# Kernel optimization log

Measured on AMD Instinct MI355X. Metric: run time of the kernel, lower is better.

## Reference

```python
import jax, jax.numpy as jnp
import numpy as np

N, E, E3, DIM = 25000, 50000, 40000, 64


def setup_inputs() -> dict:
    key = jax.random.key(0)
    ks = jax.random.split(key, 16)
    def g(k, shape, scale=0.1):
        return jax.random.normal(k, shape, jnp.float32) * scale
    return {
        "x": jax.random.normal(ks[0], (N, 8), jnp.float32),
        "edge_attr": jax.random.uniform(ks[1], (E, 19), dtype=jnp.float32),
        "edge_attr3": jax.random.uniform(ks[2], (E3, 8), dtype=jnp.float32),
        "edge_index": jax.random.randint(ks[3], (2, E), 0, N),
        "edge_index3": jax.random.randint(ks[4], (2, E3), 0, N),
        "W_node": g(ks[5], (8, DIM)), "b_node": jnp.zeros((DIM,), jnp.float32),
        "W_ea": g(ks[6], (19, 12)), "b_ea": jnp.zeros((12,), jnp.float32),
        "W_e1": g(ks[7], (12, 128)), "b_e1": jnp.zeros((128,), jnp.float32),
        "W_e2": g(ks[8], (128, DIM * DIM), 0.01), "b_e2": jnp.zeros((DIM * DIM,), jnp.float32),
        "conv_bias": jnp.zeros((DIM,), jnp.float32),
        "W_ih": g(ks[9], (3 * DIM, DIM)), "b_ih": jnp.zeros((3 * DIM,), jnp.float32),
        "W_hh": g(ks[10], (3 * DIM, DIM)), "b_hh": jnp.zeros((3 * DIM,), jnp.float32),
        "W_l1": g(ks[11], (DIM + 8, 128)), "b_l1": jnp.zeros((128,), jnp.float32),
        "W_l2": g(ks[12], (128, 1)), "b_l2": jnp.zeros((1,), jnp.float32),
    }


def _forward(x, edge_attr, edge_attr3,
             W_node, b_node, W_ea, b_ea, W_e1, b_e1, W_e2, b_e2, conv_bias,
             W_ih, b_ih, W_hh, b_hh, W_l1, b_l1, W_l2, b_l2,
             edge_index, edge_index3):
    dim = W_node.shape[1]
    n = x.shape[0]
    out = jax.nn.relu(x @ W_node + b_node)                      # [N, dim]
    ea = jax.nn.relu(edge_attr @ W_ea + b_ea)                   # [E, 12]
    # edge MLP -> per-edge dim x dim weight matrices (same for all 3 conv calls)
    Wedge = (jax.nn.relu(ea @ W_e1 + b_e1) @ W_e2 + b_e2).reshape(-1, dim, dim)  # [E, dim, dim]
    src, dst = edge_index[0], edge_index[1]
    ones = jnp.ones((src.shape[0],), x.dtype)
    cnt = jnp.maximum(jax.ops.segment_sum(ones, dst, num_segments=n), 1.0)  # [N]
    h = out
    for _ in range(3):
        msg = jnp.einsum('ed,edf->ef', out[src], Wedge)                     # per-edge GEMV
        agg = jax.ops.segment_sum(msg, dst, num_segments=n) / cnt[:, None]  # scatter-mean
        m = jax.nn.relu(agg + conv_bias)
        # single-step GRU (PyTorch gate order: r, z, n)
        gi = m @ W_ih.T + b_ih
        gh = h @ W_hh.T + b_hh
        ir, iz, inn = jnp.split(gi, 3, axis=-1)
        hr, hz, hn = jnp.split(gh, 3, axis=-1)
        r = jax.nn.sigmoid(ir + hr)
        z = jax.nn.sigmoid(iz + hz)
        ng = jnp.tanh(inn + r * hn)
        h = (1.0 - z) * ng + z * h
        out = h
    pair = (out[edge_index3[0]] + out[edge_index3[1]]) * 0.5    # mean over the 2 endpoints
    yhat = jnp.concatenate([pair, edge_attr3], axis=1)          # [E3, dim+8]
    yhat = jax.nn.relu(yhat @ W_l1 + b_l1) @ W_l2 + b_l2        # [E3, 1]
    return yhat[:, 0]


def reference(x, edge_attr, edge_attr3, edge_index, edge_index3,
              W_node, b_node, W_ea, b_ea, W_e1, b_e1, W_e2, b_e2, conv_bias,
              W_ih, b_ih, W_hh, b_hh, W_l1, b_l1, W_l2, b_l2):
    return _forward(x, edge_attr, edge_attr3,
                    W_node, b_node, W_ea, b_ea, W_e1, b_e1, W_e2, b_e2, conv_bias,
                    W_ih, b_ih, W_hh, b_hh, W_l1, b_l1, W_l2, b_l2,
                    edge_index, edge_index3)
```

## Files before the change

kernel.cpp:

```cpp
#include <hip/hip_runtime.h>

typedef unsigned short u16;
typedef unsigned int u32;
typedef __attribute__((ext_vector_type(8))) short short8v;
typedef __attribute__((ext_vector_type(4))) float float4v;

__device__ __forceinline__ float sigm(float x) { return 1.0f / (1.0f + __expf(-x)); }
__device__ __forceinline__ u16 f2bf(float f) {
  u32 u = __float_as_uint(f);
  u32 r = (u + 0x7fffu + ((u >> 16) & 1u)) >> 16;
  return (u16)r;
}
__device__ __forceinline__ float bf2f(u16 w) { return __uint_as_float(((u32)w) << 16); }

__global__ void k_zero_f(float* __restrict__ p, int n) {
  int i = blockIdx.x * blockDim.x + threadIdx.x;
  if (i < n) p[i] = 0.0f;
}
__global__ void k_zero_i(int* __restrict__ p, int n) {
  int i = blockIdx.x * blockDim.x + threadIdx.x;
  if (i < n) p[i] = 0;
}

__global__ void k_cnt(const int* __restrict__ dst, int* __restrict__ cnt, int E) {
  int e = blockIdx.x * blockDim.x + threadIdx.x;
  if (e < E) atomicAdd(&cnt[dst[e]], 1);
}

__global__ void k_node(const float* __restrict__ x, const float* __restrict__ Wn,
                       const float* __restrict__ bn, float* __restrict__ h, int N) {
  int tid = blockIdx.x * blockDim.x + threadIdx.x;
  if (tid >= N * 64) return;
  int n = tid >> 6, f = tid & 63;
  float acc = bn[f];
  for (int k = 0; k < 8; ++k) acc += x[(size_t)n * 8 + k] * Wn[k * 64 + f];
  h[tid] = fmaxf(acc, 0.0f);
}

__global__ __launch_bounds__(256) void k_edge_mlp(
    const float* __restrict__ ea_in, const float* __restrict__ Wea,
    const float* __restrict__ bea, const float* __restrict__ We1,
    const float* __restrict__ be1, u16* __restrict__ Ahi, int E) {
  __shared__ float att[2][19];
  __shared__ float ea[2][12];
  int half = threadIdx.x >> 7;
  int t = threadIdx.x & 127;
  int e = blockIdx.x * 2 + half;
  bool real = (e < E);
  int ee = real ? e : E - 1;
  if (t < 19) att[half][t] = ea_in[(size_t)ee * 19 + t];
  __syncthreads();
  if (t < 12) {
    float a = bea[t];
#pragma unroll
    for (int k = 0; k < 19; ++k) a += att[half][k] * Wea[k * 12 + t];
    ea[half][t] = fmaxf(a, 0.0f);
  }
  __syncthreads();
  float a = be1[t];
#pragma unroll
  for (int j = 0; j < 12; ++j) a += ea[half][j] * We1[j * 128 + t];
  if (real) Ahi[(size_t)e * 128 + t] = f2bf(fmaxf(a, 0.0f));
}

__global__ void k_pack_b(const float* __restrict__ W2, u16* __restrict__ Bph) {
  int tid = blockIdx.x * blockDim.x + threadIdx.x;
  if (tid >= 128 * 4096) return;
  int j = tid & 7;
  int lane = (tid >> 3) & 63;
  int nt = (tid >> 9) & 3;
  int ks = (tid >> 11) & 3;
  int d = tid >> 13;
  int c = lane & 15, q = lane >> 4;
  int k = ks * 32 + q * 8 + j;
  int n = d * 64 + nt * 16 + c;
  Bph[tid] = f2bf(W2[(size_t)k * 4096 + n]);
}

__global__ void k_prep_wtf(const float* __restrict__ Wih, const float* __restrict__ Whh,
                           u16* __restrict__ WpI, u16* __restrict__ WpH) {
  int tid = blockIdx.x * blockDim.x + threadIdx.x;
  if (tid >= 2 * 12288) return;
  int w = tid / 12288;
  int r = tid - w * 12288;
  int jj = r & 7;
  int lane = (r >> 3) & 63;
  int t = r >> 9;
  int nt = t % 12, ks = t / 12;
  int c = lane & 15, q = lane >> 4;
  int j = nt * 16 + c;
  int k = ks * 32 + q * 8 + jj;
  const float* W = w ? Whh : Wih;
  u16* Wp = w ? WpH : WpI;
  Wp[r] = f2bf(W[j * 64 + k]);
}

__global__ void k_prep_wl1(const float* __restrict__ Wl1, u16* __restrict__ Wp1) {
  int tid = blockIdx.x * blockDim.x + threadIdx.x;
  if (tid >= 3 * 8 * 64 * 8) return;
  int j = tid & 7;
  int lane = (tid >> 3) & 63;
  int nt = (tid >> 9) & 7;
  int ks = tid >> 12;
  int c = lane & 15, q = lane >> 4;
  int k = ks * 32 + q * 8 + j;
  int n = nt * 16 + c;
  Wp1[tid] = f2bf((k < 72) ? Wl1[k * 128 + n] : 0.0f);
}

__global__ __launch_bounds__(256, 2) void k_conv_fused(
    const u16* __restrict__ Ahi, const u16* __restrict__ Bph,
    const float* __restrict__ b2, const float* __restrict__ h,
    const int* __restrict__ src, const int* __restrict__ dst,
    float* __restrict__ agg, int E) {
  __shared__ __align__(16) u16 sB[2][8192];
  __shared__ __align__(16) float hs[128 * 36];
  __shared__ __align__(16) float sb2[2048];
  int m0 = blockIdx.x * 128;
  int d0 = blockIdx.y * 32;
  int tid = threadIdx.x;
  int wave = tid >> 6, lane = tid & 63;
  int mw = wave >> 1, fw = wave & 1;
  int c = lane & 15, q = lane >> 4;

  auto stageB = [&](int d, int b) {
    const u16* gp = Bph + (size_t)d * 8192 + wave * 2048 + lane * 8;
    u16* lp = &sB[b][wave * 2048];
#pragma unroll
    for (int i = 0; i < 4; ++i)
      __builtin_amdgcn_global_load_lds(
          (const __attribute__((address_space(1))) unsigned int*)(gp + i * 512),
          (__attribute__((address_space(3))) unsigned int*)(lp + i * 512), 16, 0, 0);
  };

  stageB(d0, 0);

  short8v afr[4][4];
#pragma unroll
  for (int mt = 0; mt < 4; ++mt) {
    int gr = m0 + mw * 64 + mt * 16 + c;
    if (gr >= E) gr = E - 1;
    const u16* ap = Ahi + (size_t)gr * 128 + q * 8;
#pragma unroll
    for (int ks = 0; ks < 4; ++ks) afr[mt][ks] = *(const short8v*)(ap + ks * 32);
  }

#pragma unroll
  for (int p = 0; p < 4; ++p) {
    int slot = p * 256 + tid;
    int r = slot >> 3, s = slot & 7;
    int ge = m0 + r;
    if (ge >= E) ge = E - 1;
    int sn = src[ge];
    *(float4*)(&hs[r * 36 + s * 4]) = *(const float4*)(h + (size_t)sn * 64 + d0 + s * 4);
  }
#pragma unroll
  for (int p = 0; p < 2; ++p) {
    int slot = p * 256 + tid;
    *(float4*)(&sb2[slot * 4]) = *(const float4*)(b2 + d0 * 64 + slot * 4);
  }
  __syncthreads();

  float msg[4][2][4];
#pragma unroll
  for (int mt = 0; mt < 4; ++mt)
#pragma unroll
    for (int nt = 0; nt < 2; ++nt)
#pragma unroll
      for (int r = 0; r < 4; ++r) msg[mt][nt][r] = 0.0f;

  int cur = 0;
  for (int dl = 0; dl < 32; ++dl) {
    if (dl < 31) stageB(d0 + dl + 1, cur ^ 1);
    float4v acc[4][2];
#pragma unroll
    for (int mt = 0; mt < 4; ++mt)
#pragma unroll
      for (int nt = 0; nt < 2; ++nt) acc[mt][nt] = (float4v){0.f, 0.f, 0.f, 0.f};
#pragma unroll
    for (int ks = 0; ks < 4; ++ks) {
      short8v b0 = *(const short8v*)(&sB[cur][ks * 2048 + fw * 1024 + lane * 8]);
      short8v b1 = *(const short8v*)(&sB[cur][ks * 2048 + fw * 1024 + 512 + lane * 8]);
#pragma unroll
      for (int mt = 0; mt < 4; ++mt) {
        acc[mt][0] = __builtin_amdgcn_mfma_f32_16x16x32_bf16(afr[mt][ks], b0, acc[mt][0], 0, 0, 0);
        acc[mt][1] = __builtin_amdgcn_mfma_f32_16x16x32_bf16(afr[mt][ks], b1, acc[mt][1], 0, 0, 0);
      }
    }
#pragma unroll
    for (int mt = 0; mt < 4; ++mt) {
      float hd[4];
#pragma unroll
      for (int r = 0; r < 4; ++r)
        hd[r] = hs[(mw * 64 + mt * 16 + q * 4 + r) * 36 + dl];
#pragma unroll
      for (int nt = 0; nt < 2; ++nt) {
        float b2v = sb2[dl * 64 + fw * 32 + nt * 16 + c];
#pragma unroll
        for (int r = 0; r < 4; ++r) msg[mt][nt][r] += hd[r] * (acc[mt][nt][r] + b2v);
      }
    }
    __syncthreads();
    cur ^= 1;
  }

#pragma unroll
  for (int mt = 0; mt < 4; ++mt) {
#pragma unroll
    for (int r = 0; r < 4; ++r) {
      int e = m0 + mw * 64 + mt * 16 + q * 4 + r;
      if (e < E) {
        int dn = dst[e];
        float* ap = agg + (size_t)dn * 64 + fw * 32 + c;
#pragma unroll
        for (int nt = 0; nt < 2; ++nt) atomicAdd(ap + nt * 16, msg[mt][nt][r]);
      }
    }
  }
}

__global__ __launch_bounds__(256, 2) void k_gru_mfma(
    float* __restrict__ agg, const int* __restrict__ cnt,
    const float* __restrict__ cb, const u16* __restrict__ WpI,
    const u16* __restrict__ WpH, const float* __restrict__ bih,
    const float* __restrict__ bhh, const float* __restrict__ hin,
    float* __restrict__ hout, int N) {
  __shared__ __align__(16) u16 sM[64 * 72];
  __shared__ __align__(16) u16 sH[64 * 72];
  __shared__ __align__(16) float sHf[64 * 68];
  int n0 = blockIdx.x * 64;
  int tid = threadIdx.x;
#pragma unroll
  for (int p = 0; p < 16; ++p) {
    int slot = p * 256 + tid;
    int n = slot >> 6, f = slot & 63;
    int gn = n0 + n;
    bool real = (gn < N);
    if (!real) gn = N - 1;
    float cf = fmaxf((float)cnt[gn], 1.0f);
    float av = agg[(size_t)gn * 64 + f];
    if (real) agg[(size_t)gn * 64 + f] = 0.0f;
    float m = fmaxf(av / cf + cb[f], 0.0f);
    float hv = hin[(size_t)gn * 64 + f];
    sM[n * 72 + f] = f2bf(m);
    sH[n * 72 + f] = f2bf(hv);
    sHf[n * 68 + f] = hv;
  }
  __syncthreads();
  int wave = tid >> 6, lane = tid & 63;
  int c = lane & 15, q = lane >> 4;
  short8v am[2], ah[2];
#pragma unroll
  for (int ks = 0; ks < 2; ++ks) {
    am[ks] = *(const short8v*)(&sM[(wave * 16 + c) * 72 + ks * 32 + q * 8]);
    ah[ks] = *(const short8v*)(&sH[(wave * 16 + c) * 72 + ks * 32 + q * 8]);
  }
  float4v accRZ[8], accN[4], accHN[4];
#pragma unroll
  for (int i = 0; i < 8; ++i) accRZ[i] = (float4v){0.f, 0.f, 0.f, 0.f};
#pragma unroll
  for (int i = 0; i < 4; ++i) {
    accN[i] = (float4v){0.f, 0.f, 0.f, 0.f};
    accHN[i] = (float4v){0.f, 0.f, 0.f, 0.f};
  }
#pragma unroll
  for (int ks = 0; ks < 2; ++ks) {
#pragma unroll
    for (int nt = 0; nt < 8; ++nt) {
      short8v bI = *(const short8v*)(WpI + ((size_t)(ks * 12 + nt) * 64 + lane) * 8);
      short8v bH = *(const short8v*)(WpH + ((size_t)(ks * 12 + nt) * 64 + lane) * 8);
      accRZ[nt] = __builtin_amdgcn_mfma_f32_16x16x32_bf16(am[ks], bI, accRZ[nt], 0, 0, 0);
      accRZ[nt] = __builtin_amdgcn_mfma_f32_16x16x32_bf16(ah[ks], bH, accRZ[nt], 0, 0, 0);
    }
#pragma unroll
    for (int nt = 0; nt < 4; ++nt) {
      short8v bI = *(const short8v*)(WpI + ((size_t)(ks * 12 + 8 + nt) * 64 + lane) * 8);
      short8v bH = *(const short8v*)(WpH + ((size_t)(ks * 12 + 8 + nt) * 64 + lane) * 8);
      accN[nt] = __builtin_amdgcn_mfma_f32_16x16x32_bf16(am[ks], bI, accN[nt], 0, 0, 0);
      accHN[nt] = __builtin_amdgcn_mfma_f32_16x16x32_bf16(ah[ks], bH, accHN[nt], 0, 0, 0);
    }
  }
#pragma unroll
  for (int nt = 0; nt < 4; ++nt) {
    int f = nt * 16 + c;
    float brz_r = bih[f] + bhh[f];
    float brz_z = bih[64 + f] + bhh[64 + f];
    float bin = bih[128 + f];
    float bhn = bhh[128 + f];
#pragma unroll
    for (int r = 0; r < 4; ++r) {
      int nl = wave * 16 + q * 4 + r;
      int gn = n0 + nl;
      float rr = sigm(accRZ[nt][r] + brz_r);
      float zz = sigm(accRZ[nt + 4][r] + brz_z);
      float ng = tanhf(accN[nt][r] + bin + rr * (accHN[nt][r] + bhn));
      float hv = sHf[nl * 68 + f];
      if (gn < N) hout[(size_t)gn * 64 + f] = (1.0f - zz) * ng + zz * hv;
    }
  }
}

__global__ __launch_bounds__(256) void k_final_mfma(
    const float* __restrict__ h, const float* __restrict__ ea3,
    const int* __restrict__ idx3, const u16* __restrict__ Wp1,
    const float* __restrict__ bl1, const float* __restrict__ Wl2,
    const float* __restrict__ bl2, float* __restrict__ out, int E3) {
  __shared__ __align__(16) u16 sF[64 * 104];
  int e0 = blockIdx.x * 64;
  int tid = threadIdx.x;
  {
    int er = tid >> 2;
    int part = tid & 3;
    int ge = e0 + er;
    int gc = (ge < E3) ? ge : E3 - 1;
    int a = idx3[gc], b = idx3[E3 + gc];
    for (int kk = part * 24; kk < part * 24 + 24; ++kk) {
      float v;
      if (kk < 64) v = 0.5f * (h[(size_t)a * 64 + kk] + h[(size_t)b * 64 + kk]);
      else if (kk < 72) v = ea3[(size_t)gc * 8 + (kk - 64)];
      else v = 0.0f;
      sF[er * 104 + kk] = f2bf(v);
    }
  }
  __syncthreads();
  int wave = tid >> 6, lane = tid & 63;
  int c = lane & 15, q = lane >> 4;
  float4v acc[8];
#pragma unroll
  for (int nt = 0; nt < 8; ++nt) acc[nt] = (float4v){0.f, 0.f, 0.f, 0.f};
#pragma unroll
  for (int ks = 0; ks < 3; ++ks) {
    short8v af = *(const short8v*)(&sF[(wave * 16 + c) * 104 + ks * 32 + q * 8]);
#pragma unroll
    for (int nt = 0; nt < 8; ++nt) {
      short8v bf = *(const short8v*)(Wp1 + ((size_t)(ks * 8 + nt) * 64 + lane) * 8);
      acc[nt] = __builtin_amdgcn_mfma_f32_16x16x32_bf16(af, bf, acc[nt], 0, 0, 0);
    }
  }
  float v[4] = {0.f, 0.f, 0.f, 0.f};
#pragma unroll
  for (int nt = 0; nt < 8; ++nt) {
    int n = nt * 16 + c;
    float b1 = bl1[n];
    float w2 = Wl2[n];
#pragma unroll
    for (int r = 0; r < 4; ++r) v[r] += fmaxf(acc[nt][r] + b1, 0.0f) * w2;
  }
#pragma unroll
  for (int off = 1; off < 16; off <<= 1) {
#pragma unroll
    for (int r = 0; r < 4; ++r) v[r] += __shfl_xor(v[r], off);
  }
  if (c == 0) {
    float b2v = bl2[0];
#pragma unroll
    for (int r = 0; r < 4; ++r) {
      int e = e0 + wave * 16 + q * 4 + r;
      if (e < E3) out[e] = v[r] + b2v;
    }
  }
}

extern "C" void kernel_launch(void* const* d_in, const int* in_sizes, int n_in,
                              void* d_out, int out_size, void* d_ws, size_t ws_size,
                              hipStream_t stream) {
  const float* x          = (const float*)d_in[0];
  const float* edge_attr  = (const float*)d_in[1];
  const float* edge_attr3 = (const float*)d_in[2];
  const int*   edge_index = (const int*)d_in[3];
  const int*   edge_index3= (const int*)d_in[4];
  const float* W_node = (const float*)d_in[5];
  const float* b_node = (const float*)d_in[6];
  const float* W_ea   = (const float*)d_in[7];
  const float* b_ea   = (const float*)d_in[8];
  const float* W_e1   = (const float*)d_in[9];
  const float* b_e1   = (const float*)d_in[10];
  const float* W_e2   = (const float*)d_in[11];
  const float* b_e2   = (const float*)d_in[12];
  const float* conv_bias = (const float*)d_in[13];
  const float* W_ih   = (const float*)d_in[14];
  const float* b_ih   = (const float*)d_in[15];
  const float* W_hh   = (const float*)d_in[16];
  const float* b_hh   = (const float*)d_in[17];
  const float* W_l1   = (const float*)d_in[18];
  const float* b_l1   = (const float*)d_in[19];
  const float* W_l2   = (const float*)d_in[20];
  const float* b_l2   = (const float*)d_in[21];

  int N  = in_sizes[0] / 8;
  int E  = in_sizes[1] / 19;
  int E3 = in_sizes[2] / 8;

  char* p = (char*)d_ws;
  auto carve = [&](size_t bytes) -> void* {
    char* q = p;
    p += (bytes + 255) & ~(size_t)255;
    return (void*)q;
  };
  float* hA   = (float*)carve((size_t)N * 64 * 4);
  float* hB   = (float*)carve((size_t)N * 64 * 4);
  float* agg  = (float*)carve((size_t)N * 64 * 4);
  int*   cnt  = (int*)carve((size_t)N * 4);
  u16*   Ahi  = (u16*)carve((size_t)E * 128 * 2);
  u16*   Bph  = (u16*)carve((size_t)128 * 4096 * 2);
  u16*   WpI  = (u16*)carve(12288 * 2);
  u16*   WpH  = (u16*)carve(12288 * 2);
  u16*   Wp1  = (u16*)carve(12288 * 2);

  const int* src = edge_index;
  const int* dst = edge_index + E;

  k_zero_i<<<(N + 255) / 256, 256, 0, stream>>>(cnt, N);
  k_cnt<<<(E + 255) / 256, 256, 0, stream>>>(dst, cnt, E);
  k_node<<<((size_t)N * 64 + 255) / 256, 256, 0, stream>>>(x, W_node, b_node, hA, N);
  k_edge_mlp<<<(E + 1) / 2, 256, 0, stream>>>(edge_attr, W_ea, b_ea, W_e1, b_e1, Ahi, E);
  k_pack_b<<<(128 * 4096 + 255) / 256, 256, 0, stream>>>(W_e2, Bph);
  k_prep_wtf<<<(2 * 12288 + 255) / 256, 256, 0, stream>>>(W_ih, W_hh, WpI, WpH);
  k_prep_wl1<<<(12288 + 255) / 256, 256, 0, stream>>>(W_l1, Wp1);
  k_zero_f<<<((size_t)N * 64 + 255) / 256, 256, 0, stream>>>(agg, N * 64);

  float* hcur = hA;
  float* hnxt = hB;
  dim3 gconv((E + 127) / 128, 2);
  int ngru = (N + 63) / 64;
  for (int it = 0; it < 3; ++it) {
    k_conv_fused<<<gconv, 256, 0, stream>>>(Ahi, Bph, b_e2, hcur, src, dst, agg, E);
    k_gru_mfma<<<ngru, 256, 0, stream>>>(agg, cnt, conv_bias, WpI, WpH,
                                         b_ih, b_hh, hcur, hnxt, N);
    float* tmp = hcur; hcur = hnxt; hnxt = tmp;
  }
  k_final_mfma<<<(E3 + 63) / 64, 256, 0, stream>>>(hcur, edge_attr3, edge_index3, Wp1,
                                                   b_l1, W_l2, b_l2, (float*)d_out, E3);
}
```

Measured before the change: 466.1 us.

## Replace atomic scatter with CSR gather and merge conv d-split blocks

The conv kernel no longer splits the 64 input features across two blocks. Each block now loops over all 64 d slices and writes per-edge messages densely to a message buffer instead of atomically adding into per-node aggregates. A CSR (counting scan plus permutation) built once per call lets the GRU kernel gather and average each node's messages directly, which removes the agg zeroing and the float atomics. In exchange there is an extra E×64 message buffer round trip per iteration and a single-block serial scan. The per-block conv work doubles while the grid halves, and the bias is now stored as bf16 in LDS, which changes the numerics slightly.

```diff
diff --git a/kernel.cpp b/kernel.cpp
--- a/kernel.cpp
+++ b/kernel.cpp
@@ -13,10 +13,6 @@
 }
 __device__ __forceinline__ float bf2f(u16 w) { return __uint_as_float(((u32)w) << 16); }
 
-__global__ void k_zero_f(float* __restrict__ p, int n) {
-  int i = blockIdx.x * blockDim.x + threadIdx.x;
-  if (i < n) p[i] = 0.0f;
-}
 __global__ void k_zero_i(int* __restrict__ p, int n) {
   int i = blockIdx.x * blockDim.x + threadIdx.x;
   if (i < n) p[i] = 0;
@@ -25,6 +21,41 @@
 __global__ void k_cnt(const int* __restrict__ dst, int* __restrict__ cnt, int E) {
   int e = blockIdx.x * blockDim.x + threadIdx.x;
   if (e < E) atomicAdd(&cnt[dst[e]], 1);
+}
+
+__global__ void k_scan(const int* __restrict__ cnt, int* __restrict__ row, int N) {
+  __shared__ int part[256];
+  __shared__ int base[256];
+  int t = threadIdx.x;
+  int chunk = (N + 255) >> 8;
+  int s0 = t * chunk;
+  int s1 = min(s0 + chunk, N);
+  int s = 0;
+  for (int i = s0; i < s1; ++i) s += cnt[i];
+  part[t] = s;
+  __syncthreads();
+  if (t == 0) {
+    int run = 0;
+    for (int i = 0; i < 256; ++i) { int v = part[i]; base[i] = run; run += v; }
+  }
+  __syncthreads();
+  int run = base[t];
+  for (int i = s0; i < s1; ++i) { row[i] = run; run += cnt[i]; }
+  if (t == 255) row[N] = run;
+}
+
+__global__ void k_copy_i(const int* __restrict__ a, int* __restrict__ b, int n) {
+  int i = blockIdx.x * blockDim.x + threadIdx.x;
+  if (i < n) b[i] = a[i];
+}
+
+__global__ void k_perm(const int* __restrict__ dst, int* __restrict__ cursor,
+                       int* __restrict__ perm, int E) {
+  int e = blockIdx.x * blockDim.x + threadIdx.x;
+  if (e < E) {
+    int p = atomicAdd(&cursor[dst[e]], 1);
+    perm[p] = e;
+  }
 }
 
 __global__ void k_node(const float* __restrict__ x, const float* __restrict__ Wn,
@@ -111,13 +142,11 @@
 __global__ __launch_bounds__(256, 2) void k_conv_fused(
     const u16* __restrict__ Ahi, const u16* __restrict__ Bph,
     const float* __restrict__ b2, const float* __restrict__ h,
-    const int* __restrict__ src, const int* __restrict__ dst,
-    float* __restrict__ agg, int E) {
+    const int* __restrict__ src, float* __restrict__ msgout, int E) {
   __shared__ __align__(16) u16 sB[2][8192];
-  __shared__ __align__(16) float hs[128 * 36];
-  __shared__ __align__(16) float sb2[2048];
+  __shared__ __align__(16) float hs[128 * 68];
+  __shared__ __align__(16) u16 sb2h[4096];
   int m0 = blockIdx.x * 128;
-  int d0 = blockIdx.y * 32;
   int tid = threadIdx.x;
   int wave = tid >> 6, lane = tid & 63;
   int mw = wave >> 1, fw = wave & 1;
@@ -133,7 +162,7 @@
           (__attribute__((address_space(3))) unsigned int*)(lp + i * 512), 16, 0, 0);
   };
 
-  stageB(d0, 0);
+  stageB(0, 0);
 
   short8v afr[4][4];
 #pragma unroll
@@ -146,18 +175,24 @@
   }
 
 #pragma unroll
-  for (int p = 0; p < 4; ++p) {
+  for (int p = 0; p < 8; ++p) {
     int slot = p * 256 + tid;
-    int r = slot >> 3, s = slot & 7;
+    int r = slot >> 4, s = slot & 15;
     int ge = m0 + r;
     if (ge >= E) ge = E - 1;
     int sn = src[ge];
-    *(float4*)(&hs[r * 36 + s * 4]) = *(const float4*)(h + (size_t)sn * 64 + d0 + s * 4);
-  }
-#pragma unroll
-  for (int p = 0; p < 2; ++p) {
-    int slot = p * 256 + tid;
-    *(float4*)(&sb2[slot * 4]) = *(const float4*)(b2 + d0 * 64 + slot * 4);
+    *(float4*)(&hs[r * 68 + s * 4]) = *(const float4*)(h + (size_t)sn * 64 + s * 4);
+  }
+  {
+    int t16 = tid * 16;
+#pragma unroll
+    for (int u = 0; u < 4; ++u) {
+      float4 v = *(const float4*)(b2 + t16 + u * 4);
+      sb2h[t16 + u * 4 + 0] = f2bf(v.x);
+      sb2h[t16 + u * 4 + 1] = f2bf(v.y);
+      sb2h[t16 + u * 4 + 2] = f2bf(v.z);
+      sb2h[t16 + u * 4 + 3] = f2bf(v.w);
+    }
   }
   __syncthreads();
 
@@ -170,8 +205,8 @@
       for (int r = 0; r < 4; ++r) msg[mt][nt][r] = 0.0f;
 
   int cur = 0;
-  for (int dl = 0; dl < 32; ++dl) {
-    if (dl < 31) stageB(d0 + dl + 1, cur ^ 1);
+  for (int dl = 0; dl < 64; ++dl) {
+    if (dl < 63) stageB(dl + 1, cur ^ 1);
     float4v acc[4][2];
 #pragma unroll
     for (int mt = 0; mt < 4; ++mt)
@@ -192,10 +227,10 @@
       float hd[4];
 #pragma unroll
       for (int r = 0; r < 4; ++r)
-        hd[r] = hs[(mw * 64 + mt * 16 + q * 4 + r) * 36 + dl];
+        hd[r] = hs[(mw * 64 + mt * 16 + q * 4 + r) * 68 + dl];
 #pragma unroll
       for (int nt = 0; nt < 2; ++nt) {
-        float b2v = sb2[dl * 64 + fw * 32 + nt * 16 + c];
+        float b2v = bf2f(sb2h[dl * 64 + fw * 32 + nt * 16 + c]);
 #pragma unroll
         for (int r = 0; r < 4; ++r) msg[mt][nt][r] += hd[r] * (acc[mt][nt][r] + b2v);
       }
@@ -210,21 +245,20 @@
     for (int r = 0; r < 4; ++r) {
       int e = m0 + mw * 64 + mt * 16 + q * 4 + r;
       if (e < E) {
-        int dn = dst[e];
-        float* ap = agg + (size_t)dn * 64 + fw * 32 + c;
-#pragma unroll
-        for (int nt = 0; nt < 2; ++nt) atomicAdd(ap + nt * 16, msg[mt][nt][r]);
+        float* mp = msgout + (size_t)e * 64 + fw * 32 + c;
+#pragma unroll
+        for (int nt = 0; nt < 2; ++nt) mp[nt * 16] = msg[mt][nt][r];
       }
     }
   }
 }
 
 __global__ __launch_bounds__(256, 2) void k_gru_mfma(
-    float* __restrict__ agg, const int* __restrict__ cnt,
-    const float* __restrict__ cb, const u16* __restrict__ WpI,
-    const u16* __restrict__ WpH, const float* __restrict__ bih,
-    const float* __restrict__ bhh, const float* __restrict__ hin,
-    float* __restrict__ hout, int N) {
+    const float* __restrict__ msg, const int* __restrict__ perm,
+    const int* __restrict__ row, const float* __restrict__ cb,
+    const u16* __restrict__ WpI, const u16* __restrict__ WpH,
+    const float* __restrict__ bih, const float* __restrict__ bhh,
+    const float* __restrict__ hin, float* __restrict__ hout, int N) {
   __shared__ __align__(16) u16 sM[64 * 72];
   __shared__ __align__(16) u16 sH[64 * 72];
   __shared__ __align__(16) float sHf[64 * 68];
@@ -235,11 +269,11 @@
     int slot = p * 256 + tid;
     int n = slot >> 6, f = slot & 63;
     int gn = n0 + n;
-    bool real = (gn < N);
-    if (!real) gn = N - 1;
-    float cf = fmaxf((float)cnt[gn], 1.0f);
-    float av = agg[(size_t)gn * 64 + f];
-    if (real) agg[(size_t)gn * 64 + f] = 0.0f;
+    if (gn >= N) gn = N - 1;
+    int b0 = row[gn], b1 = row[gn + 1];
+    float av = 0.0f;
+    for (int j = b0; j < b1; ++j) av += msg[(size_t)perm[j] * 64 + f];
+    float cf = fmaxf((float)(b1 - b0), 1.0f);
     float m = fmaxf(av / cf + cb[f], 0.0f);
     float hv = hin[(size_t)gn * 64 + f];
     sM[n * 72 + f] = f2bf(m);
@@ -397,35 +431,41 @@
     p += (bytes + 255) & ~(size_t)255;
     return (void*)q;
   };
-  float* hA   = (float*)carve((size_t)N * 64 * 4);
-  float* hB   = (float*)carve((size_t)N * 64 * 4);
-  float* agg  = (float*)carve((size_t)N * 64 * 4);
-  int*   cnt  = (int*)carve((size_t)N * 4);
-  u16*   Ahi  = (u16*)carve((size_t)E * 128 * 2);
-  u16*   Bph  = (u16*)carve((size_t)128 * 4096 * 2);
-  u16*   WpI  = (u16*)carve(12288 * 2);
-  u16*   WpH  = (u16*)carve(12288 * 2);
-  u16*   Wp1  = (u16*)carve(12288 * 2);
+  float* hA    = (float*)carve((size_t)N * 64 * 4);
+  float* hB    = (float*)carve((size_t)N * 64 * 4);
+  float* msg   = (float*)carve((size_t)E * 64 * 4);
+  int*   cnt   = (int*)carve((size_t)N * 4);
+  int*   row   = (int*)carve((size_t)(N + 1) * 4);
+  int*   cursor= (int*)carve((size_t)N * 4);
+  int*   perm  = (int*)carve((size_t)E * 4);
+  u16*   Ahi   = (u16*)carve((size_t)E * 128 * 2);
+  u16*   Bph   = (u16*)carve((size_t)128 * 4096 * 2);
+  u16*   WpI   = (u16*)carve(12288 * 2);
+  u16*   WpH   = (u16*)carve(12288 * 2);
+  u16*   Wp1   = (u16*)carve(12288 * 2);
 
   const int* src = edge_index;
   const int* dst = edge_index + E;
 
   k_zero_i<<<(N + 255) / 256, 256, 0, stream>>>(cnt, N);
   k_cnt<<<(E + 255) / 256, 256, 0, stream>>>(dst, cnt, E);
+  k_scan<<<1, 256, 0, stream>>>(cnt, row, N);
+  k_copy_i<<<(N + 255) / 256, 256, 0, stream>>>(row, cursor, N);
+  k_perm<<<(E + 255) / 256, 256, 0, stream>>>(dst, cursor, perm, E);
+
   k_node<<<((size_t)N * 64 + 255) / 256, 256, 0, stream>>>(x, W_node, b_node, hA, N);
   k_edge_mlp<<<(E + 1) / 2, 256, 0, stream>>>(edge_attr, W_ea, b_ea, W_e1, b_e1, Ahi, E);
   k_pack_b<<<(128 * 4096 + 255) / 256, 256, 0, stream>>>(W_e2, Bph);
   k_prep_wtf<<<(2 * 12288 + 255) / 256, 256, 0, stream>>>(W_ih, W_hh, WpI, WpH);
   k_prep_wl1<<<(12288 + 255) / 256, 256, 0, stream>>>(W_l1, Wp1);
-  k_zero_f<<<((size_t)N * 64 + 255) / 256, 256, 0, stream>>>(agg, N * 64);
 
   float* hcur = hA;
   float* hnxt = hB;
-  dim3 gconv((E + 127) / 128, 2);
+  int gconv = (E + 127) / 128;
   int ngru = (N + 63) / 64;
   for (int it = 0; it < 3; ++it) {
-    k_conv_fused<<<gconv, 256, 0, stream>>>(Ahi, Bph, b_e2, hcur, src, dst, agg, E);
-    k_gru_mfma<<<ngru, 256, 0, stream>>>(agg, cnt, conv_bias, WpI, WpH,
+    k_conv_fused<<<gconv, 256, 0, stream>>>(Ahi, Bph, b_e2, hcur, src, msg, E);
+    k_gru_mfma<<<ngru, 256, 0, stream>>>(msg, perm, row, conv_bias, WpI, WpH,
                                          b_ih, b_hh, hcur, hnxt, N);
     float* tmp = hcur; hcur = hnxt; hnxt = tmp;
   }
```

Result: slower. 521.0 us (+11.8%).
